# Kernel optimization log

Hardware: AMD Instinct MI355X
Metric: run time of the kernel (lower is better)

Reference implementation:

```python
import jax, jax.numpy as jnp
import numpy as np

B, T, H, W, C = 2, 4, 128, 128, 192
HEADS = 6
WS = 8          # attention window (per-frame, wsD=1)
OW = 12         # overlapping KV window: 8 + int(8*0.5)
PAD = (OW - WS) // 2
TBL = (WS + OW - 1) ** 2   # 361 relative-position-bias entries
MLP_HID = C * 2


def setup_inputs() -> dict:
    key = jax.random.key(0)
    ks = jax.random.split(key, 8)
    s = 0.02
    return dict(
        x=jax.random.normal(ks[0], (B, T, H, W, C), jnp.float32),
        x_size=jnp.array([H, W], jnp.int32),  # unused by forward (shadowed), kept for signature fidelity
        rpi_oca=jax.random.randint(ks[1], (WS * WS, OW * OW), 0, TBL),
        norm1_g=jnp.ones((C,), jnp.float32), norm1_b=jnp.zeros((C,), jnp.float32),
        qkv_w=jax.random.normal(ks[2], (C, 3 * C), jnp.float32) * s,
        qkv_b=jnp.zeros((3 * C,), jnp.float32),
        rpb_table=jax.random.normal(ks[3], (TBL, HEADS), jnp.float32) * s,
        norm2_g=jnp.ones((C,), jnp.float32), norm2_b=jnp.zeros((C,), jnp.float32),
        fc1_w=jax.random.normal(ks[4], (C, MLP_HID), jnp.float32) * s,
        fc1_b=jnp.zeros((MLP_HID,), jnp.float32),
        fc2_w=jax.random.normal(ks[5], (MLP_HID, C), jnp.float32) * s,
        fc2_b=jnp.zeros((C,), jnp.float32),
    )


def _ln(x, g, b):
    m = x.mean(-1, keepdims=True)
    v = ((x - m) ** 2).mean(-1, keepdims=True)
    return (x - m) * jax.lax.rsqrt(v + 1e-5) * g + b


def reference(x, x_size, rpi_oca, norm1_g, norm1_b, qkv_w, qkv_b, rpb_table,
              norm2_g, norm2_b, fc1_w, fc1_b, fc2_w, fc2_b):
    b, t, h, w, c = x.shape
    d = c // HEADS
    scale = d ** -0.5
    nH, nW = h // WS, w // WS
    b_ = b * t * nH * nW  # total windows
    shortcut = x
    xn = _ln(x, norm1_g, norm1_b)
    qkv = (xn @ qkv_w + qkv_b).reshape(b, t, h, w, 3, c)
    q, k, v = qkv[..., 0, :], qkv[..., 1, :], qkv[..., 2, :]
    # --- query: non-overlapping (1,8,8) windows -> (b_, heads, 64, d)
    qw = (q.reshape(b, t, nH, WS, nW, WS, c)
           .transpose(0, 1, 2, 4, 3, 5, 6)
           .reshape(b_, WS * WS, HEADS, d)
           .transpose(0, 2, 1, 3))
    # --- key/value: overlapping (1,12,12) windows with stride 8, zero-padded by 2
    hid = (jnp.arange(nH) * WS)[:, None] + jnp.arange(OW)  # (nH, OW)
    wid = (jnp.arange(nW) * WS)[:, None] + jnp.arange(OW)  # (nW, OW)

    def owin(z):
        zp = jnp.pad(z, ((0, 0), (0, 0), (PAD, PAD), (PAD, PAD), (0, 0)))
        zw = zp[:, :, hid][:, :, :, :, wid]  # (b, t, nH, OW, nW, OW, c)
        return (zw.transpose(0, 1, 2, 4, 3, 5, 6)
                  .reshape(b_, OW * OW, HEADS, d)
                  .transpose(0, 2, 1, 3))

    kw, vw = owin(k), owin(v)
    attn = jnp.einsum('bhqd,bhkd->bhqk', qw * scale, kw)  # (b_, heads, 64, 144)
    bias = rpb_table[rpi_oca.reshape(-1)].reshape(WS * WS, OW * OW, HEADS).transpose(2, 0, 1)
    attn = attn + bias[None]  # NOTE: original forward applies NO softmax (self.softmax unused)
    out = (jnp.einsum('bhqk,bhkd->bhqd', attn, vw)
             .transpose(0, 2, 1, 3)
             .reshape(b_, WS * WS, c))
    # window_reverse
    xa = (out.reshape(b, t, nH, nW, WS, WS, c)
             .transpose(0, 1, 2, 4, 3, 5, 6)
             .reshape(b, t, h, w, c))
    x = xa + shortcut  # self.proj is never applied in the original forward
    hmlp = jax.nn.gelu(_ln(x, norm2_g, norm2_b) @ fc1_w + fc1_b, approximate=False)
    return x + (hmlp @ fc2_w + fc2_b)
```

## Files before the change

### kernel.cpp

```cpp
#include <hip/hip_runtime.h>
#include <cstdint>
#include <cstddef>

typedef short bf16x8 __attribute__((ext_vector_type(8)));
typedef unsigned short u16x4 __attribute__((ext_vector_type(4)));
typedef float f32x4  __attribute__((ext_vector_type(4)));
typedef unsigned short u16;

#define DEVI __device__ __forceinline__

constexpr int C     = 192;
constexpr int HEADS = 6;
constexpr int NQKV  = 576;
constexpr int HID   = 384;
constexpr int NTOK  = 131072;

DEVI u16 f2bf(float f){
  union { float f; unsigned u; } v; v.f = f;
  return (u16)((v.u + 0x7fffu + ((v.u >> 16) & 1u)) >> 16);
}
DEVI float bf2f(u16 h){
  union { unsigned u; float f; } v; v.u = ((unsigned)h) << 16;
  return v.f;
}
DEVI unsigned cvtpk(float a, float b){
  unsigned r;
  asm("v_cvt_pk_bf16_f32 %0, %1, %2" : "=v"(r) : "v"(a), "v"(b));
  return r;
}

DEVI float gelu(float x){
  const float e = __expf(-1.702f * x);
  const float r = __builtin_amdgcn_rcpf(1.f + e);
  return x * r;
}

__global__ void prep_kernel(const float* __restrict__ qkv_w,
                            const float* __restrict__ fc1_w,
                            const float* __restrict__ fc2_w,
                            const int*   __restrict__ rpi,
                            const float* __restrict__ rpb,
                            u16* __restrict__ qkvP,
                            u16* __restrict__ fc1P,
                            u16* __restrict__ fc2P,
                            float* __restrict__ bias_pk){
  int idx = blockIdx.x * blockDim.x + threadIdx.x;
  int stride = gridDim.x * blockDim.x;
  for(int i = idx; i < 36*6*64*8; i += stride){
    int e = i & 7, lane = (i >> 3) & 63, t = i >> 9;
    int ks = t % 6, p = t / 6;
    int n = p*16 + (lane & 15), k = ks*32 + (lane >> 4)*8 + e;
    qkvP[i] = f2bf(qkv_w[k*NQKV + n]);
  }
  for(int i = idx; i < 24*6*64*8; i += stride){
    int e = i & 7, lane = (i >> 3) & 63, t = i >> 9;
    int ks = t % 6, p = t / 6;
    int n = p*16 + (lane & 15), k = ks*32 + (lane >> 4)*8 + e;
    fc1P[i] = f2bf(fc1_w[k*HID + n]);
  }
  for(int i = idx; i < 12*12*64*8; i += stride){
    int e = i & 7, lane = (i >> 3) & 63, t = i >> 9;
    int ks = t % 12, p = t / 12;
    int n = p*16 + (lane & 15), k = ks*32 + (lane >> 4)*8 + e;
    fc2P[i] = f2bf(fc2_w[k*C + n]);
  }
  const int n4 = HEADS*5*2*4*64*4;
  for(int i = idx; i < n4; i += stride){
    int t = i;
    int r    = t & 3;  t >>= 2;
    int lane = t & 63; t >>= 6;
    int mi   = t & 3;  t >>= 2;
    int nf   = t & 1;  t >>= 1;
    int chunk = t % 5; int head = t / 5;
    int q  = mi*16 + (lane & 15);
    int kk = chunk*32 + nf*16 + ((lane >> 4) << 2) + r;
    float v = 0.f;
    if(kk < 144) v = rpb[rpi[q*144 + kk]*HEADS + head];
    bias_pk[i] = v;
  }
}

__global__ __launch_bounds__(384, 4)
void qkv_kernel(const float* __restrict__ x,
                const float* __restrict__ g1,
                const float* __restrict__ b1,
                const u16* __restrict__ wP,
                const float* __restrict__ qb,
                u16* __restrict__ qkv){
  __shared__ u16 xn[64][200];
  __shared__ u16 rp[64][152];
  const int tid = threadIdx.x;
  const int bid = blockIdx.x;
  const int nh = (bid >> 3) & 1;
  const int tb = (bid & 7) + ((bid >> 4) << 3);
  const size_t tok0 = (size_t)tb * 64;
  if(tid < 256){
    const int trow = tid >> 2;
    const int j = tid & 3;
    const float* xr = x + (tok0 + trow)*C;
    float4 xv[12];
    #pragma unroll
    for(int u = 0; u < 12; ++u)
      xv[u] = *reinterpret_cast<const float4*>(xr + u*16 + j*4);
    float s1 = 0.f, s2 = 0.f;
    #pragma unroll
    for(int u = 0; u < 12; ++u){
      const float* f = reinterpret_cast<const float*>(&xv[u]);
      #pragma unroll
      for(int e = 0; e < 4; ++e){ s1 += f[e]; s2 += f[e]*f[e]; }
    }
    s1 += __shfl_xor(s1, 1, 64); s2 += __shfl_xor(s2, 1, 64);
    s1 += __shfl_xor(s1, 2, 64); s2 += __shfl_xor(s2, 2, 64);
    const float mean = s1 * (1.f/192.f);
    const float rstd = rsqrtf(s2*(1.f/192.f) - mean*mean + 1e-5f);
    #pragma unroll
    for(int u = 0; u < 12; ++u){
      const float4 gv = *reinterpret_cast<const float4*>(g1 + u*16 + j*4);
      const float4 bv = *reinterpret_cast<const float4*>(b1 + u*16 + j*4);
      const float* f = reinterpret_cast<const float*>(&xv[u]);
      const float* gp = reinterpret_cast<const float*>(&gv);
      const float* bp = reinterpret_cast<const float*>(&bv);
      float c0 = (f[0] - mean)*rstd*gp[0] + bp[0];
      float c1 = (f[1] - mean)*rstd*gp[1] + bp[1];
      float c2 = (f[2] - mean)*rstd*gp[2] + bp[2];
      float c3 = (f[3] - mean)*rstd*gp[3] + bp[3];
      uint2 pk; pk.x = cvtpk(c0, c1); pk.y = cvtpk(c2, c3);
      *reinterpret_cast<uint2*>(&xn[trow][u*16 + j*4]) = pk;
    }
  }
  __syncthreads();
  const int lane = tid & 63;
  const int wn = tid >> 6;
  const int g = lane >> 4, col = lane & 15;
  const f32x4 fzero = {0.f, 0.f, 0.f, 0.f};
  f32x4 acc[4][3];
  #pragma unroll
  for(int mi = 0; mi < 4; ++mi)
    #pragma unroll
    for(int nf = 0; nf < 3; ++nf) acc[mi][nf] = fzero;
  const int p0 = nh*18 + wn*3;
  #pragma unroll
  for(int ks = 0; ks < 6; ++ks){
    bf16x8 wf[3];
    #pragma unroll
    for(int nf = 0; nf < 3; ++nf)
      wf[nf] = *reinterpret_cast<const bf16x8*>(wP + ((size_t)(((p0 + nf)*6 + ks)*64) + lane)*8);
    bf16x8 a[4];
    #pragma unroll
    for(int mi = 0; mi < 4; ++mi)
      a[mi] = *reinterpret_cast<const bf16x8*>(&xn[mi*16 + col][ks*32 + g*8]);
    #pragma unroll
    for(int nf = 0; nf < 3; ++nf)
      #pragma unroll
      for(int mi = 0; mi < 4; ++mi)
        acc[mi][nf] = __builtin_amdgcn_mfma_f32_16x16x32_bf16(a[mi], wf[nf], acc[mi][nf], 0, 0, 0);
  }
  #pragma unroll
  for(int ph = 0; ph < 2; ++ph){
    if(wn >= ph*3 && wn < ph*3 + 3){
      const int wl = wn - ph*3;
      #pragma unroll
      for(int mi = 0; mi < 4; ++mi){
        #pragma unroll
        for(int nf = 0; nf < 3; ++nf){
          const int nloc = wl*48 + nf*16 + col;
          const float bb = qb[nh*288 + ph*144 + nloc];
          const int row0 = mi*16 + g*4;
          const unsigned p01 = cvtpk(acc[mi][nf][0] + bb, acc[mi][nf][1] + bb);
          const unsigned p23 = cvtpk(acc[mi][nf][2] + bb, acc[mi][nf][3] + bb);
          rp[row0 + 0][nloc] = (u16)p01;
          rp[row0 + 1][nloc] = (u16)(p01 >> 16);
          rp[row0 + 2][nloc] = (u16)p23;
          rp[row0 + 3][nloc] = (u16)(p23 >> 16);
        }
      }
    }
    __syncthreads();
    #pragma unroll
    for(int it = 0; it < 3; ++it){
      const int c = tid + it*384;
      const int tok = c / 18, cc = c - tok*18;
      const int n0 = nh*288 + ph*144 + cc*8;
      const int pl = n0 >> 5, d0 = n0 & 31;
      bf16x8 vv = *reinterpret_cast<const bf16x8*>(&rp[tok][cc*8]);
      *reinterpret_cast<bf16x8*>(qkv + ((size_t)pl*NTOK + tok0 + tok)*32 + d0) = vv;
    }
    __syncthreads();
  }
}

template<bool X1B>
__global__ __launch_bounds__(256, 5)
void attn_kernel(const u16* __restrict__ qkv,
                 const float* __restrict__ bias_pk,
                 const float* __restrict__ x,
                 float* __restrict__ out,
                 u16* __restrict__ x1b){
  __shared__ alignas(16) char smem[28672];
  u16 (*Kl)[40]  = reinterpret_cast<u16(*)[40]>(smem);
  u16 (*Vt)[168] = reinterpret_cast<u16(*)[168]>(smem + 12800);
  char* Plb      = smem + 23552;
  float (*Of)[36] = reinterpret_cast<float(*)[36]>(smem);
  const int tid  = threadIdx.x;
  const int lane = tid & 63;
  const int w    = tid >> 6;
  const int g = lane >> 4, col = lane & 15;
  const int win = blockIdx.x, head = blockIdx.y;
  const int bt = win >> 8, wh = (win >> 4) & 15, ww = win & 15;
  const int h0 = wh*8, w0 = ww*8;
  const size_t tokbase = (size_t)bt * 16384;
  const u16* Qp = qkv + (size_t)head      *NTOK*32;
  const u16* Kp = qkv + (size_t)(6 + head)*NTOK*32;
  const u16* Vp = qkv + (size_t)(12 + head)*NTOK*32;
  const bf16x8 z8 = {0,0,0,0,0,0,0,0};

  #pragma unroll
  for(int ii = 0; ii < 3; ++ii){
    const int i = w + ii*4;
    if(i < 10){
      const int kr = i*16 + col;
      const int r12 = (kr*2731) >> 15;
      const int c12 = kr - r12*12;
      const int hh = h0 - 2 + r12;
      const int wp = w0 - 2 + c12;
      const bool valid = (kr < 144) && (hh >= 0) && (hh < 128) && (wp >= 0) && (wp < 128);
      const size_t t = valid ? (tokbase + (size_t)hh*128 + wp) : tokbase;
      bf16x8 kv_ = *reinterpret_cast<const bf16x8*>(Kp + t*32 + g*8);
      bf16x8 vv_ = *reinterpret_cast<const bf16x8*>(Vp + t*32 + g*8);
      kv_ = valid ? kv_ : z8;
      vv_ = valid ? vv_ : z8;
      *reinterpret_cast<bf16x8*>(&Kl[kr][g*8]) = kv_;
      #pragma unroll
      for(int e = 0; e < 8; ++e) Vt[g*8 + e][kr] = (u16)vv_[e];
    }
  }
  bf16x8 qf;
  {
    const int row = w*16 + col;
    const size_t t = tokbase + (size_t)(h0 + (row >> 3))*128 + (w0 + (row & 7));
    qf = *reinterpret_cast<const bf16x8*>(Qp + t*32 + g*8);
  }
  __syncthreads();

  const f32x4 fzero = {0.f, 0.f, 0.f, 0.f};
  f32x4 oacc[2];
  oacc[0] = fzero; oacc[1] = fzero;
  const float scale = 0.17677669529663689f;

  #pragma unroll
  for(int ch = 0; ch < 5; ++ch){
    float4 bv[2];
    #pragma unroll
    for(int nf = 0; nf < 2; ++nf)
      bv[nf] = *reinterpret_cast<const float4*>(
          bias_pk + (size_t)((((head*5 + ch)*2 + nf)*4 + w)*64 + lane)*4);
    bf16x8 kfr[2];
    #pragma unroll
    for(int nf = 0; nf < 2; ++nf)
      kfr[nf] = *reinterpret_cast<const bf16x8*>(&Kl[ch*32 + nf*16 + col][g*8]);
    f32x4 st[2];
    #pragma unroll
    for(int nf = 0; nf < 2; ++nf)
      st[nf] = __builtin_amdgcn_mfma_f32_16x16x32_bf16(kfr[nf], qf, fzero, 0, 0, 0);
    #pragma unroll
    for(int nf = 0; nf < 2; ++nf){
      const float* bp = reinterpret_cast<const float*>(&bv[nf]);
      const float p0 = fmaf(st[nf][0], scale, bp[0]);
      const float p1 = fmaf(st[nf][1], scale, bp[1]);
      const float p2 = fmaf(st[nf][2], scale, bp[2]);
      const float p3 = fmaf(st[nf][3], scale, bp[3]);
      uint2 pw;
      pw.x = cvtpk(p0, p1);
      pw.y = cvtpk(p2, p3);
      *reinterpret_cast<uint2*>(Plb + (w*16 + col)*80 + nf*32 + g*8) = pw;
    }
    bf16x8 pa = *reinterpret_cast<const bf16x8*>(Plb + (w*16 + col)*80 + g*16);
    bf16x8 vfr[2];
    #pragma unroll
    for(int nf = 0; nf < 2; ++nf)
      vfr[nf] = *reinterpret_cast<const bf16x8*>(&Vt[nf*16 + col][ch*32 + g*8]);
    #pragma unroll
    for(int nf = 0; nf < 2; ++nf)
      oacc[nf] = __builtin_amdgcn_mfma_f32_16x16x32_bf16(pa, vfr[nf], oacc[nf], 0, 0, 0);
  }
  __syncthreads();
  #pragma unroll
  for(int nf = 0; nf < 2; ++nf)
    #pragma unroll
    for(int r = 0; r < 4; ++r)
      Of[w*16 + g*4 + r][nf*16 + col] = oacc[nf][r];
  __syncthreads();
  {
    const int tok = tid >> 2, q = tid & 3;
    const int hh = h0 + (tok >> 3), wp = w0 + (tok & 7);
    const size_t trow = tokbase + (size_t)hh*128 + wp;
    const size_t o = trow*(size_t)C + head*32 + q*8;
    float4 a0 = *reinterpret_cast<const float4*>(&Of[tok][q*8]);
    float4 a1 = *reinterpret_cast<const float4*>(&Of[tok][q*8 + 4]);
    const float4 x0 = *reinterpret_cast<const float4*>(x + o);
    const float4 x1 = *reinterpret_cast<const float4*>(x + o + 4);
    a0.x += x0.x; a0.y += x0.y; a0.z += x0.z; a0.w += x0.w;
    a1.x += x1.x; a1.y += x1.y; a1.z += x1.z; a1.w += x1.w;
    if(X1B){
      uint4 pk;
      pk.x = cvtpk(a0.x, a0.y);
      pk.y = cvtpk(a0.z, a0.w);
      pk.z = cvtpk(a1.x, a1.y);
      pk.w = cvtpk(a1.z, a1.w);
      *reinterpret_cast<uint4*>(x1b + o) = pk;
    }else{
      *reinterpret_cast<float4*>(out + o)     = a0;
      *reinterpret_cast<float4*>(out + o + 4) = a1;
    }
  }
}

template<bool X1B>
__global__ __launch_bounds__(256, 4)
void mlp_kernel(float* __restrict__ io,
                const u16* __restrict__ x1b,
                const float* __restrict__ g2,
                const float* __restrict__ b2,
                const u16* __restrict__ w1P,
                const float* __restrict__ fb1,
                const u16* __restrict__ w2P,
                const float* __restrict__ fb2){
  __shared__ u16 xn[32][200];
  __shared__ u16 hl[32][392];
  const int tid = threadIdx.x;
  const size_t tok0 = (size_t)blockIdx.x * 32;
  {
    const int trow = tid >> 3;
    const int j = tid & 7;
    float v[24];
    if(X1B){
      const u16* xr = x1b + (tok0 + trow)*C + j*24;
      bf16x8 b0 = *reinterpret_cast<const bf16x8*>(xr);
      bf16x8 b1 = *reinterpret_cast<const bf16x8*>(xr + 8);
      bf16x8 b2_ = *reinterpret_cast<const bf16x8*>(xr + 16);
      #pragma unroll
      for(int e = 0; e < 8; ++e){ v[e] = bf2f((u16)b0[e]); v[8+e] = bf2f((u16)b1[e]); v[16+e] = bf2f((u16)b2_[e]); }
    }else{
      const float* xr = io + (tok0 + trow)*C + j*24;
      #pragma unroll
      for(int u = 0; u < 6; ++u){
        const float4 t = *reinterpret_cast<const float4*>(xr + u*4);
        v[u*4+0] = t.x; v[u*4+1] = t.y; v[u*4+2] = t.z; v[u*4+3] = t.w;
      }
    }
    float s1 = 0.f, s2 = 0.f;
    #pragma unroll
    for(int e = 0; e < 24; ++e){ s1 += v[e]; s2 += v[e]*v[e]; }
    s1 += __shfl_xor(s1, 1, 64); s2 += __shfl_xor(s2, 1, 64);
    s1 += __shfl_xor(s1, 2, 64); s2 += __shfl_xor(s2, 2, 64);
    s1 += __shfl_xor(s1, 4, 64); s2 += __shfl_xor(s2, 4, 64);
    const float mean = s1 * (1.f/192.f);
    const float rstd = rsqrtf(s2*(1.f/192.f) - mean*mean + 1e-5f);
    #pragma unroll
    for(int u = 0; u < 6; ++u){
      const float4 gv = *reinterpret_cast<const float4*>(g2 + j*24 + u*4);
      const float4 bv = *reinterpret_cast<const float4*>(b2 + j*24 + u*4);
      const float* gp = reinterpret_cast<const float*>(&gv);
      const float* bp = reinterpret_cast<const float*>(&bv);
      float c0 = (v[u*4+0] - mean)*rstd*gp[0] + bp[0];
      float c1 = (v[u*4+1] - mean)*rstd*gp[1] + bp[1];
      float c2 = (v[u*4+2] - mean)*rstd*gp[2] + bp[2];
      float c3 = (v[u*4+3] - mean)*rstd*gp[3] + bp[3];
      uint2 pk; pk.x = cvtpk(c0, c1); pk.y = cvtpk(c2, c3);
      *reinterpret_cast<uint2*>(&xn[trow][j*24 + u*4]) = pk;
    }
  }
  __syncthreads();
  const int lane = tid & 63, w = tid >> 6;
  const int g = lane >> 4, col = lane & 15;
  const f32x4 fzero = {0.f, 0.f, 0.f, 0.f};
  f32x4 acc1[2][6];
  #pragma unroll
  for(int mi = 0; mi < 2; ++mi)
    #pragma unroll
    for(int nf = 0; nf < 6; ++nf) acc1[mi][nf] = fzero;
  #pragma unroll
  for(int ks = 0; ks < 6; ++ks){
    bf16x8 wf[6];
    #pragma unroll
    for(int nf = 0; nf < 6; ++nf)
      wf[nf] = *reinterpret_cast<const bf16x8*>(w1P + ((size_t)(((w*6 + nf)*6 + ks)*64) + lane)*8);
    bf16x8 a[2];
    #pragma unroll
    for(int mi = 0; mi < 2; ++mi)
      a[mi] = *reinterpret_cast<const bf16x8*>(&xn[mi*16 + col][ks*32 + g*8]);
    #pragma unroll
    for(int nf = 0; nf < 6; ++nf)
      #pragma unroll
      for(int mi = 0; mi < 2; ++mi)
        acc1[mi][nf] = __builtin_amdgcn_mfma_f32_16x16x32_bf16(a[mi], wf[nf], acc1[mi][nf], 0, 0, 0);
  }
  #pragma unroll
  for(int mi = 0; mi < 2; ++mi){
    #pragma unroll
    for(int nf = 0; nf < 6; ++nf){
      const int nl = w*96 + nf*16 + col;
      const float bb = fb1[nl];
      const int row0 = mi*16 + g*4;
      const unsigned p01 = cvtpk(gelu(acc1[mi][nf][0] + bb), gelu(acc1[mi][nf][1] + bb));
      const unsigned p23 = cvtpk(gelu(acc1[mi][nf][2] + bb), gelu(acc1[mi][nf][3] + bb));
      hl[row0 + 0][nl] = (u16)p01;
      hl[row0 + 1][nl] = (u16)(p01 >> 16);
      hl[row0 + 2][nl] = (u16)p23;
      hl[row0 + 3][nl] = (u16)(p23 >> 16);
    }
  }
  __syncthreads();
  f32x4 acc2[2][3];
  #pragma unroll
  for(int mi = 0; mi < 2; ++mi)
    #pragma unroll
    for(int nf = 0; nf < 3; ++nf) acc2[mi][nf] = fzero;
  #pragma unroll
  for(int ks = 0; ks < 12; ++ks){
    bf16x8 wf[3];
    #pragma unroll
    for(int nf = 0; nf < 3; ++nf)
      wf[nf] = *reinterpret_cast<const bf16x8*>(w2P + ((size_t)(((w*3 + nf)*12 + ks)*64) + lane)*8);
    bf16x8 a[2];
    #pragma unroll
    for(int mi = 0; mi < 2; ++mi)
      a[mi] = *reinterpret_cast<const bf16x8*>(&hl[mi*16 + col][ks*32 + g*8]);
    #pragma unroll
    for(int nf = 0; nf < 3; ++nf)
      #pragma unroll
      for(int mi = 0; mi < 2; ++mi)
        acc2[mi][nf] = __builtin_amdgcn_mfma_f32_16x16x32_bf16(a[mi], wf[nf], acc2[mi][nf], 0, 0, 0);
  }
  if(X1B){
    #pragma unroll
    for(int mi = 0; mi < 2; ++mi){
      #pragma unroll
      for(int nf = 0; nf < 3; ++nf){
        const int n = w*48 + nf*16 + col;
        const float bb = fb2[n];
        const int row0 = mi*16 + g*4;
        const unsigned p01 = cvtpk(acc2[mi][nf][0] + bb, acc2[mi][nf][1] + bb);
        const unsigned p23 = cvtpk(acc2[mi][nf][2] + bb, acc2[mi][nf][3] + bb);
        xn[row0 + 0][n] = (u16)p01;
        xn[row0 + 1][n] = (u16)(p01 >> 16);
        xn[row0 + 2][n] = (u16)p23;
        xn[row0 + 3][n] = (u16)(p23 >> 16);
      }
    }
    __syncthreads();
    const int trow = tid >> 3, j = tid & 7;
    const u16* xq = x1b + (tok0 + trow)*C + j*24;
    float* op = io + (tok0 + trow)*C + j*24;
    bf16x8 r0 = *reinterpret_cast<const bf16x8*>(xq);
    bf16x8 r1 = *reinterpret_cast<const bf16x8*>(xq + 8);
    bf16x8 r2 = *reinterpret_cast<const bf16x8*>(xq + 16);
    bf16x8 m0 = *reinterpret_cast<const bf16x8*>(&xn[trow][j*24]);
    bf16x8 m1 = *reinterpret_cast<const bf16x8*>(&xn[trow][j*24 + 8]);
    bf16x8 m2 = *reinterpret_cast<const bf16x8*>(&xn[trow][j*24 + 16]);
    float ov[24];
    #pragma unroll
    for(int e = 0; e < 8; ++e){
      ov[e]    = bf2f((u16)r0[e]) + bf2f((u16)m0[e]);
      ov[8+e]  = bf2f((u16)r1[e]) + bf2f((u16)m1[e]);
      ov[16+e] = bf2f((u16)r2[e]) + bf2f((u16)m2[e]);
    }
    #pragma unroll
    for(int u = 0; u < 6; ++u){
      float4 t; t.x = ov[u*4]; t.y = ov[u*4+1]; t.z = ov[u*4+2]; t.w = ov[u*4+3];
      *reinterpret_cast<float4*>(op + u*4) = t;
    }
  }else{
    #pragma unroll
    for(int mi = 0; mi < 2; ++mi){
      #pragma unroll
      for(int nf = 0; nf < 3; ++nf){
        const int n = w*48 + nf*16 + col;
        const float bb = fb2[n];
        #pragma unroll
        for(int r = 0; r < 4; ++r){
          const int row = mi*16 + g*4 + r;
          const size_t idx = (tok0 + row)*C + n;
          io[idx] = acc2[mi][nf][r] + bb + io[idx];
        }
      }
    }
  }
}

extern "C" void kernel_launch(void* const* d_in, const int* in_sizes, int n_in,
                              void* d_out, int out_size, void* d_ws, size_t ws_size,
                              hipStream_t stream){
  const float* x    = (const float*)d_in[0];
  const int*   rpi  = (const int*)  d_in[2];
  const float* n1g  = (const float*)d_in[3];
  const float* n1b  = (const float*)d_in[4];
  const float* qkvw = (const float*)d_in[5];
  const float* qkvb = (const float*)d_in[6];
  const float* rpb  = (const float*)d_in[7];
  const float* n2g  = (const float*)d_in[8];
  const float* n2b  = (const float*)d_in[9];
  const float* fc1w = (const float*)d_in[10];
  const float* fc1b = (const float*)d_in[11];
  const float* fc2w = (const float*)d_in[12];
  const float* fc2b = (const float*)d_in[13];
  float* out = (float*)d_out;
  char* ws = (char*)d_ws;
  u16*   qkvP    = (u16*)  (ws + 0);
  u16*   fc1P    = (u16*)  (ws + 221184);
  u16*   fc2P    = (u16*)  (ws + 368640);
  float* bias_pk = (float*)(ws + 516096);
  u16*   qkvbuf  = (u16*)  (ws + 1499136);
  u16*   x1b     = (u16*)  (ws + 152494080);
  if(ws_size < 152494080ull) return;
  const bool big = ws_size >= 202825728ull;
  prep_kernel<<<dim3(512), dim3(256), 0, stream>>>(qkvw, fc1w, fc2w, rpi, rpb, qkvP, fc1P, fc2P, bias_pk);
  qkv_kernel<<<dim3(4096), dim3(384), 0, stream>>>(x, n1g, n1b, qkvP, qkvb, qkvbuf);
  if(big){
    attn_kernel<true><<<dim3(2048, 6), dim3(256), 0, stream>>>(qkvbuf, bias_pk, x, out, x1b);
    mlp_kernel<true><<<dim3(4096), dim3(256), 0, stream>>>(out, x1b, n2g, n2b, fc1P, fc1b, fc2P, fc2b);
  }else{
    attn_kernel<false><<<dim3(2048, 6), dim3(256), 0, stream>>>(qkvbuf, bias_pk, x, out, nullptr);
    mlp_kernel<false><<<dim3(4096), dim3(256), 0, stream>>>(out, nullptr, n2g, n2b, fc1P, fc1b, fc2P, fc2b);
  }
}
```

Baseline: 261.7 us.

## Split fused MLP into separate fc1 and fc2 kernels via bf16 hidden buffer

On the large-workspace path, the fused LN2+fc1+GELU+fc2 kernel is replaced by two kernels. fc1_kernel handles 64 tokens per block with 6 waves and writes the GELU hidden activations as bf16 into the reused qkv buffer. fc2_kernel reads them back, does the second GEMM and the residual add. This aims for larger tiles and better weight reuse and occupancy in each GEMM, at the cost of an extra global round trip of the hidden tensor and one more launch.

Measured after the change: 291.0 us. 11.2% more time.

```diff
diff --git a/kernel.cpp b/kernel.cpp
--- a/kernel.cpp
+++ b/kernel.cpp
@@ -315,10 +315,192 @@
   }
 }
 
-template<bool X1B>
+__global__ __launch_bounds__(384, 3)
+void fc1_kernel(const u16* __restrict__ x1b,
+                const float* __restrict__ g2,
+                const float* __restrict__ b2,
+                const u16* __restrict__ w1P,
+                const float* __restrict__ fb1,
+                u16* __restrict__ hid){
+  __shared__ u16 xn[64][200];
+  __shared__ u16 rp[64][200];
+  const int tid = threadIdx.x;
+  const size_t tok0 = (size_t)blockIdx.x * 64;
+  if(tid < 256){
+    const int trow = tid >> 2;
+    const int j = tid & 3;
+    const u16* xr = x1b + (tok0 + trow)*C + j*48;
+    float v[48];
+    #pragma unroll
+    for(int u = 0; u < 6; ++u){
+      bf16x8 b8 = *reinterpret_cast<const bf16x8*>(xr + u*8);
+      #pragma unroll
+      for(int e = 0; e < 8; ++e) v[u*8 + e] = bf2f((u16)b8[e]);
+    }
+    float s1 = 0.f, s2 = 0.f;
+    #pragma unroll
+    for(int e = 0; e < 48; ++e){ s1 += v[e]; s2 += v[e]*v[e]; }
+    s1 += __shfl_xor(s1, 1, 64); s2 += __shfl_xor(s2, 1, 64);
+    s1 += __shfl_xor(s1, 2, 64); s2 += __shfl_xor(s2, 2, 64);
+    const float mean = s1 * (1.f/192.f);
+    const float rstd = rsqrtf(s2*(1.f/192.f) - mean*mean + 1e-5f);
+    #pragma unroll
+    for(int u = 0; u < 12; ++u){
+      const float4 gv = *reinterpret_cast<const float4*>(g2 + j*48 + u*4);
+      const float4 bv = *reinterpret_cast<const float4*>(b2 + j*48 + u*4);
+      const float* gp = reinterpret_cast<const float*>(&gv);
+      const float* bp = reinterpret_cast<const float*>(&bv);
+      float c0 = (v[u*4+0] - mean)*rstd*gp[0] + bp[0];
+      float c1 = (v[u*4+1] - mean)*rstd*gp[1] + bp[1];
+      float c2 = (v[u*4+2] - mean)*rstd*gp[2] + bp[2];
+      float c3 = (v[u*4+3] - mean)*rstd*gp[3] + bp[3];
+      uint2 pk; pk.x = cvtpk(c0, c1); pk.y = cvtpk(c2, c3);
+      *reinterpret_cast<uint2*>(&xn[trow][j*48 + u*4]) = pk;
+    }
+  }
+  __syncthreads();
+  const int lane = tid & 63;
+  const int wn = tid >> 6;
+  const int g = lane >> 4, col = lane & 15;
+  const f32x4 fzero = {0.f, 0.f, 0.f, 0.f};
+  f32x4 acc[4][4];
+  #pragma unroll
+  for(int mi = 0; mi < 4; ++mi)
+    #pragma unroll
+    for(int nf = 0; nf < 4; ++nf) acc[mi][nf] = fzero;
+  #pragma unroll
+  for(int ks = 0; ks < 6; ++ks){
+    bf16x8 wf[4];
+    #pragma unroll
+    for(int nf = 0; nf < 4; ++nf)
+      wf[nf] = *reinterpret_cast<const bf16x8*>(w1P + ((size_t)(((wn*4 + nf)*6 + ks)*64) + lane)*8);
+    bf16x8 a[4];
+    #pragma unroll
+    for(int mi = 0; mi < 4; ++mi)
+      a[mi] = *reinterpret_cast<const bf16x8*>(&xn[mi*16 + col][ks*32 + g*8]);
+    #pragma unroll
+    for(int nf = 0; nf < 4; ++nf)
+      #pragma unroll
+      for(int mi = 0; mi < 4; ++mi)
+        acc[mi][nf] = __builtin_amdgcn_mfma_f32_16x16x32_bf16(a[mi], wf[nf], acc[mi][nf], 0, 0, 0);
+  }
+  #pragma unroll
+  for(int ph = 0; ph < 2; ++ph){
+    if(wn >= ph*3 && wn < ph*3 + 3){
+      #pragma unroll
+      for(int mi = 0; mi < 4; ++mi){
+        #pragma unroll
+        for(int nf = 0; nf < 4; ++nf){
+          const int ng = wn*64 + nf*16 + col;
+          const int nl = ng - ph*192;
+          const float bb = fb1[ng];
+          const int row0 = mi*16 + g*4;
+          const unsigned p01 = cvtpk(gelu(acc[mi][nf][0] + bb), gelu(acc[mi][nf][1] + bb));
+          const unsigned p23 = cvtpk(gelu(acc[mi][nf][2] + bb), gelu(acc[mi][nf][3] + bb));
+          rp[row0 + 0][nl] = (u16)p01;
+          rp[row0 + 1][nl] = (u16)(p01 >> 16);
+          rp[row0 + 2][nl] = (u16)p23;
+          rp[row0 + 3][nl] = (u16)(p23 >> 16);
+        }
+      }
+    }
+    __syncthreads();
+    #pragma unroll
+    for(int it = 0; it < 4; ++it){
+      const int c = tid + it*384;
+      const int tok = c / 24, cc = c - tok*24;
+      bf16x8 vv = *reinterpret_cast<const bf16x8*>(&rp[tok][cc*8]);
+      *reinterpret_cast<bf16x8*>(hid + (tok0 + tok)*HID + ph*192 + cc*8) = vv;
+    }
+    __syncthreads();
+  }
+}
+
+__global__ __launch_bounds__(256, 4)
+void fc2_kernel(float* __restrict__ out,
+                const u16* __restrict__ x1b,
+                const u16* __restrict__ w2P,
+                const float* __restrict__ fb2,
+                const u16* __restrict__ hid){
+  __shared__ u16 hl[32][392];
+  __shared__ u16 xo[32][200];
+  const int tid = threadIdx.x;
+  const size_t tok0 = (size_t)blockIdx.x * 32;
+  {
+    const int trow = tid >> 3, j = tid & 7;
+    const u16* hr = hid + (tok0 + trow)*HID + j*48;
+    #pragma unroll
+    for(int u = 0; u < 6; ++u)
+      *reinterpret_cast<bf16x8*>(&hl[trow][j*48 + u*8]) = *reinterpret_cast<const bf16x8*>(hr + u*8);
+  }
+  __syncthreads();
+  const int lane = tid & 63, w = tid >> 6;
+  const int g = lane >> 4, col = lane & 15;
+  const f32x4 fzero = {0.f, 0.f, 0.f, 0.f};
+  f32x4 acc2[2][3];
+  #pragma unroll
+  for(int mi = 0; mi < 2; ++mi)
+    #pragma unroll
+    for(int nf = 0; nf < 3; ++nf) acc2[mi][nf] = fzero;
+  #pragma unroll
+  for(int ks = 0; ks < 12; ++ks){
+    bf16x8 wf[3];
+    #pragma unroll
+    for(int nf = 0; nf < 3; ++nf)
+      wf[nf] = *reinterpret_cast<const bf16x8*>(w2P + ((size_t)(((w*3 + nf)*12 + ks)*64) + lane)*8);
+    bf16x8 a[2];
+    #pragma unroll
+    for(int mi = 0; mi < 2; ++mi)
+      a[mi] = *reinterpret_cast<const bf16x8*>(&hl[mi*16 + col][ks*32 + g*8]);
+    #pragma unroll
+    for(int nf = 0; nf < 3; ++nf)
+      #pragma unroll
+      for(int mi = 0; mi < 2; ++mi)
+        acc2[mi][nf] = __builtin_amdgcn_mfma_f32_16x16x32_bf16(a[mi], wf[nf], acc2[mi][nf], 0, 0, 0);
+  }
+  #pragma unroll
+  for(int mi = 0; mi < 2; ++mi){
+    #pragma unroll
+    for(int nf = 0; nf < 3; ++nf){
+      const int n = w*48 + nf*16 + col;
+      const float bb = fb2[n];
+      const int row0 = mi*16 + g*4;
+      const unsigned p01 = cvtpk(acc2[mi][nf][0] + bb, acc2[mi][nf][1] + bb);
+      const unsigned p23 = cvtpk(acc2[mi][nf][2] + bb, acc2[mi][nf][3] + bb);
+      xo[row0 + 0][n] = (u16)p01;
+      xo[row0 + 1][n] = (u16)(p01 >> 16);
+      xo[row0 + 2][n] = (u16)p23;
+      xo[row0 + 3][n] = (u16)(p23 >> 16);
+    }
+  }
+  __syncthreads();
+  {
+    const int trow = tid >> 3, j = tid & 7;
+    const u16* xq = x1b + (tok0 + trow)*C + j*24;
+    float* op = out + (tok0 + trow)*C + j*24;
+    bf16x8 r0 = *reinterpret_cast<const bf16x8*>(xq);
+    bf16x8 r1 = *reinterpret_cast<const bf16x8*>(xq + 8);
+    bf16x8 r2 = *reinterpret_cast<const bf16x8*>(xq + 16);
+    bf16x8 m0 = *reinterpret_cast<const bf16x8*>(&xo[trow][j*24]);
+    bf16x8 m1 = *reinterpret_cast<const bf16x8*>(&xo[trow][j*24 + 8]);
+    bf16x8 m2 = *reinterpret_cast<const bf16x8*>(&xo[trow][j*24 + 16]);
+    float ov[24];
+    #pragma unroll
+    for(int e = 0; e < 8; ++e){
+      ov[e]    = bf2f((u16)r0[e]) + bf2f((u16)m0[e]);
+      ov[8+e]  = bf2f((u16)r1[e]) + bf2f((u16)m1[e]);
+      ov[16+e] = bf2f((u16)r2[e]) + bf2f((u16)m2[e]);
+    }
+    #pragma unroll
+    for(int u = 0; u < 6; ++u){
+      float4 t; t.x = ov[u*4]; t.y = ov[u*4+1]; t.z = ov[u*4+2]; t.w = ov[u*4+3];
+      *reinterpret_cast<float4*>(op + u*4) = t;
+    }
+  }
+}
+
 __global__ __launch_bounds__(256, 4)
 void mlp_kernel(float* __restrict__ io,
-                const u16* __restrict__ x1b,
                 const float* __restrict__ g2,
                 const float* __restrict__ b2,
                 const u16* __restrict__ w1P,
@@ -333,20 +515,11 @@
     const int trow = tid >> 3;
     const int j = tid & 7;
     float v[24];
-    if(X1B){
-      const u16* xr = x1b + (tok0 + trow)*C + j*24;
-      bf16x8 b0 = *reinterpret_cast<const bf16x8*>(xr);
-      bf16x8 b1 = *reinterpret_cast<const bf16x8*>(xr + 8);
-      bf16x8 b2_ = *reinterpret_cast<const bf16x8*>(xr + 16);
-      #pragma unroll
-      for(int e = 0; e < 8; ++e){ v[e] = bf2f((u16)b0[e]); v[8+e] = bf2f((u16)b1[e]); v[16+e] = bf2f((u16)b2_[e]); }
-    }else{
-      const float* xr = io + (tok0 + trow)*C + j*24;
-      #pragma unroll
-      for(int u = 0; u < 6; ++u){
-        const float4 t = *reinterpret_cast<const float4*>(xr + u*4);
-        v[u*4+0] = t.x; v[u*4+1] = t.y; v[u*4+2] = t.z; v[u*4+3] = t.w;
-      }
+    const float* xr = io + (tok0 + trow)*C + j*24;
+    #pragma unroll
+    for(int u = 0; u < 6; ++u){
+      const float4 t = *reinterpret_cast<const float4*>(xr + u*4);
+      v[u*4+0] = t.x; v[u*4+1] = t.y; v[u*4+2] = t.z; v[u*4+3] = t.w;
     }
     float s1 = 0.f, s2 = 0.f;
     #pragma unroll
@@ -432,57 +605,17 @@
       for(int mi = 0; mi < 2; ++mi)
         acc2[mi][nf] = __builtin_amdgcn_mfma_f32_16x16x32_bf16(a[mi], wf[nf], acc2[mi][nf], 0, 0, 0);
   }
-  if(X1B){
-    #pragma unroll
-    for(int mi = 0; mi < 2; ++mi){
-      #pragma unroll
-      for(int nf = 0; nf < 3; ++nf){
-        const int n = w*48 + nf*16 + col;
-        const float bb = fb2[n];
-        const int row0 = mi*16 + g*4;
-        const unsigned p01 = cvtpk(acc2[mi][nf][0] + bb, acc2[mi][nf][1] + bb);
-        const unsigned p23 = cvtpk(acc2[mi][nf][2] + bb, acc2[mi][nf][3] + bb);
-        xn[row0 + 0][n] = (u16)p01;
-        xn[row0 + 1][n] = (u16)(p01 >> 16);
-        xn[row0 + 2][n] = (u16)p23;
-        xn[row0 + 3][n] = (u16)(p23 >> 16);
-      }
-    }
-    __syncthreads();
-    const int trow = tid >> 3, j = tid & 7;
-    const u16* xq = x1b + (tok0 + trow)*C + j*24;
-    float* op = io + (tok0 + trow)*C + j*24;
-    bf16x8 r0 = *reinterpret_cast<const bf16x8*>(xq);
-    bf16x8 r1 = *reinterpret_cast<const bf16x8*>(xq + 8);
-    bf16x8 r2 = *reinterpret_cast<const bf16x8*>(xq + 16);
-    bf16x8 m0 = *reinterpret_cast<const bf16x8*>(&xn[trow][j*24]);
-    bf16x8 m1 = *reinterpret_cast<const bf16x8*>(&xn[trow][j*24 + 8]);
-    bf16x8 m2 = *reinterpret_cast<const bf16x8*>(&xn[trow][j*24 + 16]);
-    float ov[24];
-    #pragma unroll
-    for(int e = 0; e < 8; ++e){
-      ov[e]    = bf2f((u16)r0[e]) + bf2f((u16)m0[e]);
-      ov[8+e]  = bf2f((u16)r1[e]) + bf2f((u16)m1[e]);
-      ov[16+e] = bf2f((u16)r2[e]) + bf2f((u16)m2[e]);
-    }
-    #pragma unroll
-    for(int u = 0; u < 6; ++u){
-      float4 t; t.x = ov[u*4]; t.y = ov[u*4+1]; t.z = ov[u*4+2]; t.w = ov[u*4+3];
-      *reinterpret_cast<float4*>(op + u*4) = t;
-    }
-  }else{
-    #pragma unroll
-    for(int mi = 0; mi < 2; ++mi){
-      #pragma unroll
-      for(int nf = 0; nf < 3; ++nf){
-        const int n = w*48 + nf*16 + col;
-        const float bb = fb2[n];
-        #pragma unroll
-        for(int r = 0; r < 4; ++r){
-          const int row = mi*16 + g*4 + r;
-          const size_t idx = (tok0 + row)*C + n;
-          io[idx] = acc2[mi][nf][r] + bb + io[idx];
-        }
+  #pragma unroll
+  for(int mi = 0; mi < 2; ++mi){
+    #pragma unroll
+    for(int nf = 0; nf < 3; ++nf){
+      const int n = w*48 + nf*16 + col;
+      const float bb = fb2[n];
+      #pragma unroll
+      for(int r = 0; r < 4; ++r){
+        const int row = mi*16 + g*4 + r;
+        const size_t idx = (tok0 + row)*C + n;
+        io[idx] = acc2[mi][nf][r] + bb + io[idx];
       }
     }
   }
@@ -512,15 +645,17 @@
   float* bias_pk = (float*)(ws + 516096);
   u16*   qkvbuf  = (u16*)  (ws + 1499136);
   u16*   x1b     = (u16*)  (ws + 152494080);
+  u16*   hid     = qkvbuf + (size_t)6*NTOK*32;
   if(ws_size < 152494080ull) return;
   const bool big = ws_size >= 202825728ull;
   prep_kernel<<<dim3(512), dim3(256), 0, stream>>>(qkvw, fc1w, fc2w, rpi, rpb, qkvP, fc1P, fc2P, bias_pk);
   qkv_kernel<<<dim3(4096), dim3(384), 0, stream>>>(x, n1g, n1b, qkvP, qkvb, qkvbuf);
   if(big){
     attn_kernel<true><<<dim3(2048, 6), dim3(256), 0, stream>>>(qkvbuf, bias_pk, x, out, x1b);
-    mlp_kernel<true><<<dim3(4096), dim3(256), 0, stream>>>(out, x1b, n2g, n2b, fc1P, fc1b, fc2P, fc2b);
+    fc1_kernel<<<dim3(2048), dim3(384), 0, stream>>>(x1b, n2g, n2b, fc1P, fc1b, hid);
+    fc2_kernel<<<dim3(4096), dim3(256), 0, stream>>>(out, x1b, fc2P, fc2b, hid);
   }else{
     attn_kernel<false><<<dim3(2048, 6), dim3(256), 0, stream>>>(qkvbuf, bias_pk, x, out, nullptr);
-    mlp_kernel<false><<<dim3(4096), dim3(256), 0, stream>>>(out, nullptr, n2g, n2b, fc1P, fc1b, fc2P, fc2b);
-  }
-}
+    mlp_kernel<<<dim3(4096), dim3(256), 0, stream>>>(out, n2g, n2b, fc1P, fc1b, fc2P, fc2b);
+  }
+}
```
